# Optimization experiments

Hardware: AMD Instinct MI355X
Metric: run time of the kernel (lower is better)

## Reference

```python
import jax, jax.numpy as jnp
import numpy as np

NP_, NT_, NG_ = 110000, 20000, 10000  # node counts per relation graph
E = 500000                              # number of interaction records / edges
D = 64                                  # embedding_dim
F_USER, F_ITEM = 16, 16                 # engineered feature dims
NUM_LAYERS = (2, 2, 2)                  # CFG.feature_num_layers


def setup_inputs() -> dict:
    key = jax.random.key(0)
    ks = jax.random.split(key, 12)
    up_edge = jax.random.randint(ks[0], (2, E), 0, NP_, dtype=jnp.int32)
    ut_edge = jax.random.randint(ks[1], (2, E), 0, NT_, dtype=jnp.int32)
    utag_edge = jax.random.randint(ks[2], (2, E), 0, NG_, dtype=jnp.int32)
    src_feat = jax.random.normal(ks[3], (E, F_USER), dtype=jnp.float32)
    dst_feat = jax.random.normal(ks[4], (E, F_ITEM), dtype=jnp.float32)
    # xavier-uniform style embedding tables
    def xavier(k, shape):
        bound = np.sqrt(6.0 / (shape[0] + shape[1])).astype(np.float32)
        return jax.random.uniform(k, shape, jnp.float32, -bound, bound)
    up_emb = xavier(ks[5], (NP_, D))
    ut_emb = xavier(ks[6], (NT_, D))
    utag_emb = xavier(ks[7], (NG_, D))
    # feature-engineering linears (stored as [in, out]; torch does x @ W.T + b)
    W_src = jax.random.normal(ks[8], (F_USER, D), dtype=jnp.float32) / np.sqrt(F_USER)
    b_src = jnp.zeros((D,), jnp.float32)
    W_dst = jax.random.normal(ks[9], (F_ITEM, D), dtype=jnp.float32) / np.sqrt(F_ITEM)
    b_dst = jnp.zeros((D,), jnp.float32)
    return dict(up_edge=up_edge, ut_edge=ut_edge, utag_edge=utag_edge,
                src_feat=src_feat, dst_feat=dst_feat,
                up_emb=up_emb, ut_emb=ut_emb, utag_emb=utag_emb,
                W_src=W_src, b_src=b_src, W_dst=W_dst, b_dst=b_dst)


def lgconv(x, edge, n):
    # PyG LGConv: symmetric-normalized propagation, no self loops, no weights.
    src, dst = edge[0], edge[1]
    ones = jnp.ones(src.shape, x.dtype)
    deg = jax.ops.segment_sum(ones, dst, num_segments=n)
    dinv = jnp.where(deg > 0, jax.lax.rsqrt(jnp.maximum(deg, 1.0)), 0.0)
    norm = dinv[src] * dinv[dst]                      # [E]
    msg = x[src] * norm[:, None]                      # gather + scale  [E, D]
    return jax.ops.segment_sum(msg, dst, num_segments=n)  # scatter-add [N, D]


def propagate(emb, edge, n_layers):
    alpha = 1.0 / (n_layers + 1)
    x = emb
    out = emb * alpha
    for _ in range(n_layers):
        x = lgconv(x, edge, emb.shape[0])
        out = out + x * alpha
    return out


def reference(up_edge, ut_edge, utag_edge, src_feat, dst_feat,
              up_emb, ut_emb, utag_emb, W_src, b_src, W_dst, b_dst):
    fs = src_feat @ W_src + b_src                     # [E, D]
    fd = dst_feat @ W_dst + b_dst                     # [E, D]
    p = propagate(up_emb, up_edge, NUM_LAYERS[0])
    t = propagate(ut_emb, ut_edge, NUM_LAYERS[1])
    g = propagate(utag_emb, utag_edge, NUM_LAYERS[2])
    # feature_aggregation_method == 0 (sum method)
    out_src = (p[up_edge[0]] + t[ut_edge[0]] + g[utag_edge[0]]) * (1.0 / 3.0) + fs
    out_dst = (p[up_edge[1]] + t[ut_edge[1]] + g[utag_edge[1]]) * (1.0 / 3.0) + fd
    return (out_src * out_dst).sum(axis=-1)           # [E] link logits
```

## Files before the change

kernel.cpp:

```cpp
#include <hip/hip_runtime.h>

#define DIM 64
#define RNG 8
#define CHK 16
#define LDSH 14336

typedef __attribute__((ext_vector_type(4))) short s16x4;
typedef __attribute__((ext_vector_type(4))) float f32x4v;

__device__ __forceinline__ float bf2f(unsigned short u) {
    union { unsigned int i; float f; } v; v.i = ((unsigned int)u) << 16; return v.f;
}
__device__ __forceinline__ unsigned short f2bf(float f) {
    union { float f; unsigned int i; } v; v.f = f;
    unsigned int r = v.i + 0x7fff + ((v.i >> 16) & 1);
    return (unsigned short)(r >> 16);
}
__device__ __forceinline__ float4 u2f4(ushort4 u) {
    float4 f; f.x = bf2f(u.x); f.y = bf2f(u.y); f.z = bf2f(u.z); f.w = bf2f(u.w);
    return f;
}
__device__ __forceinline__ ushort4 f2u4(float4 f) {
    ushort4 u; u.x = f2bf(f.x); u.y = f2bf(f.y); u.z = f2bf(f.z); u.w = f2bf(f.w);
    return u;
}
__device__ __forceinline__ float4 fma4(float4 a, float s, float4 c) {
    c.x = fmaf(a.x, s, c.x); c.y = fmaf(a.y, s, c.y);
    c.z = fmaf(a.z, s, c.z); c.w = fmaf(a.w, s, c.w);
    return c;
}
__device__ __forceinline__ float4 add4(float4 a, float4 b) {
    float4 r; r.x = a.x + b.x; r.y = a.y + b.y; r.z = a.z + b.z; r.w = a.w + b.w;
    return r;
}

__global__ __launch_bounds__(1024) void deg_cvt_kernel(
        const int* __restrict__ up, const int* __restrict__ ut,
        const int* __restrict__ ug, int* __restrict__ hist,
        const float4* __restrict__ e0, const float4* __restrict__ e1,
        const float4* __restrict__ e2, ushort4* __restrict__ embh,
        const float* __restrict__ W_s, const float* __restrict__ W_d,
        s16x4* __restrict__ wfrag,
        int NP, int NT, int NG, int NTOT, int E) {
    __shared__ int lh[LDSH];
    int b = blockIdx.x;
    const int HB = 3 * RNG * CHK;
    if (b < HB) {
        int c  = b & (CHK - 1);
        int gr = b >> 4;
        int g  = gr >> 3;
        int r  = gr & (RNG - 1);
        const int* edge = (g == 0) ? up : (g == 1) ? ut : ug;
        int nb = (g == 0) ? 0 : (g == 1) ? NP : NP + NT;
        int Ng = (g == 0) ? NP : (g == 1) ? NT : NG;
        int Q  = (Ng + RNG - 1) / RNG;
        int lo = r * Q;
        int hi = lo + Q; if (hi > Ng) hi = Ng;
        int nloc = hi - lo;
        for (int t = threadIdx.x; t < nloc; t += 1024) lh[t] = 0;
        __syncthreads();
        int CE = (E + CHK - 1) / CHK;
        int jb = c * CE, je = jb + CE; if (je > E) je = E;
        for (int j = jb + threadIdx.x; j < je; j += 1024) {
            int t = edge[E + j];
            if (t >= lo && t < hi) atomicAdd(&lh[t - lo], 1);
        }
        __syncthreads();
        for (int t = threadIdx.x; t < nloc; t += 1024)
            hist[(size_t)c * NTOT + nb + lo + t] = lh[t];
        return;
    }
    int convBlocks = (NTOT * 16 + 1023) / 1024;
    if (b >= HB + convBlocks) {
        int i = threadIdx.x;
        if (i < 512) {
            int m = i >> 8;
            int t = (i >> 6) & 3;
            int l = i & 63;
            int q = l >> 4, cc = l & 15;
            const float* Wm = m ? W_d : W_s;
            s16x4 v;
#pragma unroll
            for (int j = 0; j < 4; ++j)
                v[j] = (short)f2bf(Wm[(4 * q + j) * 64 + 4 * cc + t]);
            wfrag[i] = v;
        }
        return;
    }
    int i2 = (b - HB) * 1024 + threadIdx.x;
    int np16 = NP * 16, nt16 = NT * 16, ng16 = NG * 16;
    if (i2 >= np16 + nt16 + ng16) return;
    const float4* s; int j;
    if (i2 < np16)              { s = e0; j = i2; }
    else if (i2 < np16 + nt16)  { s = e1; j = i2 - np16; }
    else                        { s = e2; j = i2 - np16 - nt16; }
    embh[i2] = f2u4(s[j]);
}

__global__ void sumdeg_kernel(const int* __restrict__ hist, int* __restrict__ csum,
                              int* __restrict__ deg, int n) {
    int i = blockIdx.x * 256 + threadIdx.x;
    if (i >= n) return;
    int run = 0;
#pragma unroll
    for (int c = 0; c < CHK; ++c) {
        csum[(size_t)c * n + i] = run;
        run += hist[(size_t)c * n + i];
    }
    deg[i] = run;
}

__global__ void block_sums(const int* __restrict__ deg, int* __restrict__ bsum,
                           int n) {
    int i = blockIdx.x * 256 + threadIdx.x;
    int v = (i < n) ? deg[i] : 0;
#pragma unroll
    for (int s = 1; s < 64; s <<= 1) v += __shfl_xor(v, s, 64);
    __shared__ int ws[4];
    if ((threadIdx.x & 63) == 0) ws[threadIdx.x >> 6] = v;
    __syncthreads();
    if (threadIdx.x == 0) bsum[blockIdx.x] = ws[0] + ws[1] + ws[2] + ws[3];
}

__global__ void scan_bsums(int* __restrict__ bsum, int nb) {
    int lane = threadIdx.x & 63, wid = threadIdx.x >> 6;
    int v = (threadIdx.x < nb) ? bsum[threadIdx.x] : 0;
    int x = v;
#pragma unroll
    for (int s = 1; s < 64; s <<= 1) {
        int y = __shfl_up(x, s, 64);
        if (lane >= s) x += y;
    }
    __shared__ int ws[16];
    if (lane == 63) ws[wid] = x;
    __syncthreads();
    int pre = 0;
    for (int w2 = 0; w2 < wid; ++w2) pre += ws[w2];
    if (threadIdx.x < nb) bsum[threadIdx.x] = pre + x - v;
}

__global__ void scatter_offs(const int* __restrict__ deg, const int* __restrict__ bpre,
                             int* __restrict__ offs, float* __restrict__ dinv,
                             int n, int total) {
    int i = blockIdx.x * 256 + threadIdx.x;
    int lane = threadIdx.x & 63, wid = threadIdx.x >> 6;
    int v = (i < n) ? deg[i] : 0;
    int x = v;
#pragma unroll
    for (int s = 1; s < 64; s <<= 1) {
        int y = __shfl_up(x, s, 64);
        if (lane >= s) x += y;
    }
    __shared__ int ws[4];
    if (lane == 63) ws[wid] = x;
    __syncthreads();
    int pre = bpre[blockIdx.x];
    for (int w2 = 0; w2 < wid; ++w2) pre += ws[w2];
    if (i < n) {
        int e = pre + x - v;
        offs[i] = e;
        dinv[i] = (v > 0) ? rsqrtf((float)v) : 0.0f;
    }
    if (i == 0) offs[n] = total;
}

__global__ __launch_bounds__(1024) void permute3_kernel(
        const int* __restrict__ up, const int* __restrict__ ut,
        const int* __restrict__ ug, const int* __restrict__ offs,
        const int* __restrict__ csum, int* __restrict__ ei,
        int NP, int NT, int NG, int NTOT, int E) {
    __shared__ int lcur[LDSH];
    int b = blockIdx.x;
    int c  = b / 24;
    int gr = b - c * 24;
    int g  = gr >> 3;
    int r  = gr & (RNG - 1);
    const int* edge = (g == 0) ? up : (g == 1) ? ut : ug;
    int nb = (g == 0) ? 0 : (g == 1) ? NP : NP + NT;
    int Ng = (g == 0) ? NP : (g == 1) ? NT : NG;
    int Q  = (Ng + RNG - 1) / RNG;
    int lo = r * Q;
    int hi = lo + Q; if (hi > Ng) hi = Ng;
    int nloc = hi - lo;
    for (int t = threadIdx.x; t < nloc; t += 1024)
        lcur[t] = offs[nb + lo + t] + csum[(size_t)c * NTOT + nb + lo + t];
    __syncthreads();
    int CE = (E + CHK - 1) / CHK;
    int jb = c * CE, je = jb + CE; if (je > E) je = E;
    for (int j = jb + threadIdx.x; j < je; j += 1024) {
        int t = edge[E + j];
        if (t >= lo && t < hi) {
            int p = atomicAdd(&lcur[t - lo], 1);
            ei[p] = edge[j] + nb;
        }
    }
}

__global__ void conv_csr1(const int* __restrict__ offs, const int* __restrict__ ei,
                          const float* __restrict__ dinv,
                          const ushort4* __restrict__ xin, ushort4* __restrict__ xout, int N) {
    int gid = blockIdx.x * blockDim.x + threadIdx.x;
    int n = gid >> 4, l = gid & 15;
    if (n >= N) return;
    int beg = offs[n], end = offs[n + 1];
    float4 a0 = {0.f, 0.f, 0.f, 0.f}, a1 = a0, a2 = a0, a3 = a0;
    int k = beg;
    for (; k + 3 < end; k += 4) {
        int s0 = ei[k], s1 = ei[k + 1], s2 = ei[k + 2], s3 = ei[k + 3];
        float w0 = dinv[s0], w1 = dinv[s1], w2 = dinv[s2], w3 = dinv[s3];
        ushort4 u0 = xin[(size_t)s0 * 16 + l];
        ushort4 u1 = xin[(size_t)s1 * 16 + l];
        ushort4 u2 = xin[(size_t)s2 * 16 + l];
        ushort4 u3 = xin[(size_t)s3 * 16 + l];
        a0 = fma4(u2f4(u0), w0, a0);
        a1 = fma4(u2f4(u1), w1, a1);
        a2 = fma4(u2f4(u2), w2, a2);
        a3 = fma4(u2f4(u3), w3, a3);
    }
    for (; k < end; ++k) {
        int s = ei[k];
        a0 = fma4(u2f4(xin[(size_t)s * 16 + l]), dinv[s], a0);
    }
    float4 acc = add4(add4(a0, a1), add4(a2, a3));
    float sc = dinv[n];
    float4 r; r.x = acc.x * sc; r.y = acc.y * sc; r.z = acc.z * sc; r.w = acc.w * sc;
    xout[(size_t)n * 16 + l] = f2u4(r);
}

__global__ void conv_csr2(const int* __restrict__ offs, const int* __restrict__ ei,
                          const float* __restrict__ dinv,
                          const ushort4* __restrict__ emb, const ushort4* __restrict__ x1,
                          ushort4* __restrict__ out, int N) {
    int gid = blockIdx.x * blockDim.x + threadIdx.x;
    int n = gid >> 4, l = gid & 15;
    if (n >= N) return;
    int beg = offs[n], end = offs[n + 1];
    float4 a0 = {0.f, 0.f, 0.f, 0.f}, a1 = a0, a2 = a0, a3 = a0;
    int k = beg;
    for (; k + 3 < end; k += 4) {
        int s0 = ei[k], s1 = ei[k + 1], s2 = ei[k + 2], s3 = ei[k + 3];
        float w0 = dinv[s0], w1 = dinv[s1], w2 = dinv[s2], w3 = dinv[s3];
        ushort4 u0 = x1[(size_t)s0 * 16 + l];
        ushort4 u1 = x1[(size_t)s1 * 16 + l];
        ushort4 u2 = x1[(size_t)s2 * 16 + l];
        ushort4 u3 = x1[(size_t)s3 * 16 + l];
        a0 = fma4(u2f4(u0), w0, a0);
        a1 = fma4(u2f4(u1), w1, a1);
        a2 = fma4(u2f4(u2), w2, a2);
        a3 = fma4(u2f4(u3), w3, a3);
    }
    for (; k < end; ++k) {
        int s = ei[k];
        a0 = fma4(u2f4(x1[(size_t)s * 16 + l]), dinv[s], a0);
    }
    float4 acc = add4(add4(a0, a1), add4(a2, a3));
    float sc = dinv[n];
    size_t idx = (size_t)n * 16 + l;
    float4 em = u2f4(emb[idx]), x = u2f4(x1[idx]);
    const float third = 1.0f / 3.0f;
    float4 o;
    o.x = (em.x + x.x + acc.x * sc) * third;
    o.y = (em.y + x.y + acc.y * sc) * third;
    o.z = (em.z + x.z + acc.z * sc) * third;
    o.w = (em.w + x.w + acc.w * sc) * third;
    out[idx] = f2u4(o);
}

__global__ __launch_bounds__(256) void final_kernel(
        const int* __restrict__ up_e, const int* __restrict__ ut_e,
        const int* __restrict__ utag_e,
        const float* __restrict__ src_feat, const float* __restrict__ dst_feat,
        const ushort4* __restrict__ O, const s16x4* __restrict__ wfrag,
        const float4* __restrict__ b_s4, const float4* __restrict__ b_d4,
        float* __restrict__ out, int E, int NP, int NT) {
    int tid = threadIdx.x;
    int wv = tid >> 6;
    int l  = tid & 63;
    int c  = l & 15;
    int q  = l >> 4;
    int e0w = (blockIdx.x * 4 + wv) * 16;
    if (e0w >= E) return;

    int ea = e0w + c; if (ea > E - 1) ea = E - 1;
    float4 fa = *(const float4*)(src_feat + (size_t)ea * 16 + q * 4);
    float4 ga = *(const float4*)(dst_feat + (size_t)ea * 16 + q * 4);

    s16x4 Bs[4], Bd[4];
#pragma unroll
    for (int t = 0; t < 4; ++t) {
        Bs[t] = wfrag[t * 64 + l];
        Bd[t] = wfrag[256 + t * 64 + l];
    }
    float4 bsv = b_s4[c], bdv = b_d4[c];

    s16x4 As, Ad;
    As[0] = (short)f2bf(fa.x); As[1] = (short)f2bf(fa.y);
    As[2] = (short)f2bf(fa.z); As[3] = (short)f2bf(fa.w);
    Ad[0] = (short)f2bf(ga.x); Ad[1] = (short)f2bf(ga.y);
    Ad[2] = (short)f2bf(ga.z); Ad[3] = (short)f2bf(ga.w);

    ushort4 as[4][3], bs[4][3];
#pragma unroll
    for (int r = 0; r < 4; ++r) {
        int e = e0w + q * 4 + r; if (e > E - 1) e = E - 1;
        int sp = up_e[e],             dp = up_e[E + e];
        int st = ut_e[e] + NP,        dt = ut_e[E + e] + NP;
        int sg = utag_e[e] + NP + NT, dg = utag_e[E + e] + NP + NT;
        as[r][0] = O[(size_t)sp * 16 + c];
        as[r][1] = O[(size_t)st * 16 + c];
        as[r][2] = O[(size_t)sg * 16 + c];
        bs[r][0] = O[(size_t)dp * 16 + c];
        bs[r][1] = O[(size_t)dt * 16 + c];
        bs[r][2] = O[(size_t)dg * 16 + c];
    }
    __builtin_amdgcn_sched_barrier(0);

    f32x4v Cs[4], Cd[4];
    f32x4v zz = {0.f, 0.f, 0.f, 0.f};
#pragma unroll
    for (int t = 0; t < 4; ++t) {
        Cs[t] = __builtin_amdgcn_mfma_f32_16x16x16bf16_1k(As, Bs[t], zz, 0, 0, 0);
        Cd[t] = __builtin_amdgcn_mfma_f32_16x16x16bf16_1k(Ad, Bd[t], zz, 0, 0, 0);
    }

    const float third = 1.0f / 3.0f;
#pragma unroll
    for (int r = 0; r < 4; ++r) {
        int er = e0w + q * 4 + r;
        float4 fsv, fdv;
        fsv.x = Cs[0][r] + bsv.x; fsv.y = Cs[1][r] + bsv.y;
        fsv.z = Cs[2][r] + bsv.z; fsv.w = Cs[3][r] + bsv.w;
        fdv.x = Cd[0][r] + bdv.x; fdv.y = Cd[1][r] + bdv.y;
        fdv.z = Cd[2][r] + bdv.z; fdv.w = Cd[3][r] + bdv.w;
        float4 vp = u2f4(as[r][0]), vt = u2f4(as[r][1]), vg = u2f4(as[r][2]);
        float4 P, Q;
        P.x = (vp.x + vt.x + vg.x) * third + fsv.x;
        P.y = (vp.y + vt.y + vg.y) * third + fsv.y;
        P.z = (vp.z + vt.z + vg.z) * third + fsv.z;
        P.w = (vp.w + vt.w + vg.w) * third + fsv.w;
        vp = u2f4(bs[r][0]); vt = u2f4(bs[r][1]); vg = u2f4(bs[r][2]);
        Q.x = (vp.x + vt.x + vg.x) * third + fdv.x;
        Q.y = (vp.y + vt.y + vg.y) * third + fdv.y;
        Q.z = (vp.z + vt.z + vg.z) * third + fdv.z;
        Q.w = (vp.w + vt.w + vg.w) * third + fdv.w;
        float p = P.x * Q.x + P.y * Q.y + P.z * Q.z + P.w * Q.w;
        p += __shfl_xor(p, 8, 64);
        p += __shfl_xor(p, 4, 64);
        p += __shfl_xor(p, 2, 64);
        p += __shfl_xor(p, 1, 64);
        if (c == 0 && er < E) out[er] = p;
    }
}

extern "C" void kernel_launch(void* const* d_in, const int* in_sizes, int n_in,
                              void* d_out, int out_size, void* d_ws, size_t ws_size,
                              hipStream_t stream) {
    const int*   up_e     = (const int*)d_in[0];
    const int*   ut_e     = (const int*)d_in[1];
    const int*   utag_e   = (const int*)d_in[2];
    const float* src_feat = (const float*)d_in[3];
    const float* dst_feat = (const float*)d_in[4];
    const float* up_emb   = (const float*)d_in[5];
    const float* ut_emb   = (const float*)d_in[6];
    const float* utag_emb = (const float*)d_in[7];
    const float* W_src    = (const float*)d_in[8];
    const float* b_src    = (const float*)d_in[9];
    const float* W_dst    = (const float*)d_in[10];
    const float* b_dst    = (const float*)d_in[11];
    float* out = (float*)d_out;

    const int E  = in_sizes[0] / 2;
    const int NP = in_sizes[5] / DIM;
    const int NT = in_sizes[6] / DIM;
    const int NG = in_sizes[7] / DIM;
    const int NTOT = NP + NT + NG;
    const int NB = (NTOT + 255) / 256;

    char* w = (char*)d_ws;
    int*  hist = (int*)w;                       w += (size_t)CHK * NTOT * 4;
    int*  csum = (int*)w;                       w += (size_t)CHK * NTOT * 4;
    int*  deg  = (int*)w;                       w += (size_t)NTOT * 4;
    int*  offs = (int*)w;                       w += (size_t)(NTOT + 1) * 4;
    int*  bsum = (int*)w;                       w += (size_t)1024 * 4;
    float* dinv = (float*)w;                    w += (size_t)NTOT * 4;
    w = (char*)(((uintptr_t)w + 127) & ~(uintptr_t)127);
    s16x4* wfrag = (s16x4*)w;                   w += (size_t)512 * 8;
    w = (char*)(((uintptr_t)w + 127) & ~(uintptr_t)127);
    int*  ei   = (int*)w;                       w += (size_t)3 * E * 4;
    w = (char*)(((uintptr_t)w + 127) & ~(uintptr_t)127);
    ushort4* embh = (ushort4*)w;                w += (size_t)NTOT * 16 * 8;
    ushort4* x1h  = (ushort4*)w;                w += (size_t)NTOT * 16 * 8;
    ushort4* outh = (ushort4*)w;

    const int BT = 256;
    const int HB = 3 * RNG * CHK;

    {
        int convBlocks = (NTOT * 16 + 1023) / 1024;
        deg_cvt_kernel<<<dim3(HB + convBlocks + 1), dim3(1024), 0, stream>>>(
            up_e, ut_e, utag_e, hist,
            (const float4*)up_emb, (const float4*)ut_emb, (const float4*)utag_emb,
            embh, W_src, W_dst, wfrag, NP, NT, NG, NTOT, E);
    }

    sumdeg_kernel<<<dim3(NB), dim3(BT), 0, stream>>>(hist, csum, deg, NTOT);

    block_sums<<<dim3(NB), dim3(BT), 0, stream>>>(deg, bsum, NTOT);
    scan_bsums<<<dim3(1), dim3(1024), 0, stream>>>(bsum, NB);
    scatter_offs<<<dim3(NB), dim3(BT), 0, stream>>>(deg, bsum, offs, dinv, NTOT, 3 * E);

    permute3_kernel<<<dim3(CHK * 24), dim3(1024), 0, stream>>>(
        up_e, ut_e, utag_e, offs, csum, ei, NP, NT, NG, NTOT, E);

    int nb = ((size_t)NTOT * 16 + BT - 1) / BT;
    conv_csr1<<<dim3(nb), dim3(BT), 0, stream>>>(offs, ei, dinv, embh, x1h, NTOT);
    conv_csr2<<<dim3(nb), dim3(BT), 0, stream>>>(offs, ei, dinv, embh, x1h, outh, NTOT);

    {
        int blocks = (E + 63) / 64;
        final_kernel<<<dim3(blocks), dim3(BT), 0, stream>>>(
            up_e, ut_e, utag_e, src_feat, dst_feat, outh, wfrag,
            (const float4*)b_src, (const float4*)b_dst, out, E, NP, NT);
    }
}
```

Measured before the change: 329.1 us.

## Software-pipeline final kernel over four edge tiles and unroll CSR gather loops by eight

The final kernel now has each wave handle 64 edges as four 16-edge tiles. While the current tile's embedding gathers and MFMA run, it prefetches the edge indices and features for the next tile, and it loads the weight fragments once per wave instead of once per 16 edges. Separately, both CSR convolution kernels get an 8-way unrolled gather loop so more loads are in flight per thread. The cost is fewer blocks in the final kernel, which lowers parallelism, plus higher register pressure in all three kernels.

```diff
diff --git a/kernel.cpp b/kernel.cpp
--- a/kernel.cpp
+++ b/kernel.cpp
@@ -4,6 +4,7 @@
 #define RNG 8
 #define CHK 16
 #define LDSH 14336
+#define EPT 64
 
 typedef __attribute__((ext_vector_type(4))) short s16x4;
 typedef __attribute__((ext_vector_type(4))) float f32x4v;
@@ -205,6 +206,28 @@
     int beg = offs[n], end = offs[n + 1];
     float4 a0 = {0.f, 0.f, 0.f, 0.f}, a1 = a0, a2 = a0, a3 = a0;
     int k = beg;
+    for (; k + 7 < end; k += 8) {
+        int s0 = ei[k], s1 = ei[k + 1], s2 = ei[k + 2], s3 = ei[k + 3];
+        int s4 = ei[k + 4], s5 = ei[k + 5], s6 = ei[k + 6], s7 = ei[k + 7];
+        float w0 = dinv[s0], w1 = dinv[s1], w2 = dinv[s2], w3 = dinv[s3];
+        float w4 = dinv[s4], w5 = dinv[s5], w6 = dinv[s6], w7 = dinv[s7];
+        ushort4 u0 = xin[(size_t)s0 * 16 + l];
+        ushort4 u1 = xin[(size_t)s1 * 16 + l];
+        ushort4 u2 = xin[(size_t)s2 * 16 + l];
+        ushort4 u3 = xin[(size_t)s3 * 16 + l];
+        ushort4 u4 = xin[(size_t)s4 * 16 + l];
+        ushort4 u5 = xin[(size_t)s5 * 16 + l];
+        ushort4 u6 = xin[(size_t)s6 * 16 + l];
+        ushort4 u7 = xin[(size_t)s7 * 16 + l];
+        a0 = fma4(u2f4(u0), w0, a0);
+        a1 = fma4(u2f4(u1), w1, a1);
+        a2 = fma4(u2f4(u2), w2, a2);
+        a3 = fma4(u2f4(u3), w3, a3);
+        a0 = fma4(u2f4(u4), w4, a0);
+        a1 = fma4(u2f4(u5), w5, a1);
+        a2 = fma4(u2f4(u6), w6, a2);
+        a3 = fma4(u2f4(u7), w7, a3);
+    }
     for (; k + 3 < end; k += 4) {
         int s0 = ei[k], s1 = ei[k + 1], s2 = ei[k + 2], s3 = ei[k + 3];
         float w0 = dinv[s0], w1 = dinv[s1], w2 = dinv[s2], w3 = dinv[s3];
@@ -237,6 +260,28 @@
     int beg = offs[n], end = offs[n + 1];
     float4 a0 = {0.f, 0.f, 0.f, 0.f}, a1 = a0, a2 = a0, a3 = a0;
     int k = beg;
+    for (; k + 7 < end; k += 8) {
+        int s0 = ei[k], s1 = ei[k + 1], s2 = ei[k + 2], s3 = ei[k + 3];
+        int s4 = ei[k + 4], s5 = ei[k + 5], s6 = ei[k + 6], s7 = ei[k + 7];
+        float w0 = dinv[s0], w1 = dinv[s1], w2 = dinv[s2], w3 = dinv[s3];
+        float w4 = dinv[s4], w5 = dinv[s5], w6 = dinv[s6], w7 = dinv[s7];
+        ushort4 u0 = x1[(size_t)s0 * 16 + l];
+        ushort4 u1 = x1[(size_t)s1 * 16 + l];
+        ushort4 u2 = x1[(size_t)s2 * 16 + l];
+        ushort4 u3 = x1[(size_t)s3 * 16 + l];
+        ushort4 u4 = x1[(size_t)s4 * 16 + l];
+        ushort4 u5 = x1[(size_t)s5 * 16 + l];
+        ushort4 u6 = x1[(size_t)s6 * 16 + l];
+        ushort4 u7 = x1[(size_t)s7 * 16 + l];
+        a0 = fma4(u2f4(u0), w0, a0);
+        a1 = fma4(u2f4(u1), w1, a1);
+        a2 = fma4(u2f4(u2), w2, a2);
+        a3 = fma4(u2f4(u3), w3, a3);
+        a0 = fma4(u2f4(u4), w4, a0);
+        a1 = fma4(u2f4(u5), w5, a1);
+        a2 = fma4(u2f4(u6), w6, a2);
+        a3 = fma4(u2f4(u7), w7, a3);
+    }
     for (; k + 3 < end; k += 4) {
         int s0 = ei[k], s1 = ei[k + 1], s2 = ei[k + 2], s3 = ei[k + 3];
         float w0 = dinv[s0], w1 = dinv[s1], w2 = dinv[s2], w3 = dinv[s3];
@@ -278,12 +323,8 @@
     int l  = tid & 63;
     int c  = l & 15;
     int q  = l >> 4;
-    int e0w = (blockIdx.x * 4 + wv) * 16;
-    if (e0w >= E) return;
-
-    int ea = e0w + c; if (ea > E - 1) ea = E - 1;
-    float4 fa = *(const float4*)(src_feat + (size_t)ea * 16 + q * 4);
-    float4 ga = *(const float4*)(dst_feat + (size_t)ea * 16 + q * 4);
+    int wbase = (blockIdx.x * 4 + wv) * EPT;
+    if (wbase >= E) return;
 
     s16x4 Bs[4], Bd[4];
 #pragma unroll
@@ -292,63 +333,90 @@
         Bd[t] = wfrag[256 + t * 64 + l];
     }
     float4 bsv = b_s4[c], bdv = b_d4[c];
-
-    s16x4 As, Ad;
-    As[0] = (short)f2bf(fa.x); As[1] = (short)f2bf(fa.y);
-    As[2] = (short)f2bf(fa.z); As[3] = (short)f2bf(fa.w);
-    Ad[0] = (short)f2bf(ga.x); Ad[1] = (short)f2bf(ga.y);
-    Ad[2] = (short)f2bf(ga.z); Ad[3] = (short)f2bf(ga.w);
-
-    ushort4 as[4][3], bs[4][3];
+    const float third = 1.0f / 3.0f;
+
+    int ea = wbase + c; if (ea > E - 1) ea = E - 1;
+    float4 fa = *(const float4*)(src_feat + (size_t)ea * 16 + q * 4);
+    float4 ga = *(const float4*)(dst_feat + (size_t)ea * 16 + q * 4);
+    int isp[4], idp[4], ist[4], idt[4], isg[4], idg[4];
 #pragma unroll
     for (int r = 0; r < 4; ++r) {
-        int e = e0w + q * 4 + r; if (e > E - 1) e = E - 1;
-        int sp = up_e[e],             dp = up_e[E + e];
-        int st = ut_e[e] + NP,        dt = ut_e[E + e] + NP;
-        int sg = utag_e[e] + NP + NT, dg = utag_e[E + e] + NP + NT;
-        as[r][0] = O[(size_t)sp * 16 + c];
-        as[r][1] = O[(size_t)st * 16 + c];
-        as[r][2] = O[(size_t)sg * 16 + c];
-        bs[r][0] = O[(size_t)dp * 16 + c];
-        bs[r][1] = O[(size_t)dt * 16 + c];
-        bs[r][2] = O[(size_t)dg * 16 + c];
-    }
-    __builtin_amdgcn_sched_barrier(0);
-
-    f32x4v Cs[4], Cd[4];
-    f32x4v zz = {0.f, 0.f, 0.f, 0.f};
-#pragma unroll
+        int e = wbase + q * 4 + r; if (e > E - 1) e = E - 1;
+        isp[r] = up_e[e];             idp[r] = up_e[E + e];
+        ist[r] = ut_e[e] + NP;        idt[r] = ut_e[E + e] + NP;
+        isg[r] = utag_e[e] + NP + NT; idg[r] = utag_e[E + e] + NP + NT;
+    }
+
     for (int t = 0; t < 4; ++t) {
-        Cs[t] = __builtin_amdgcn_mfma_f32_16x16x16bf16_1k(As, Bs[t], zz, 0, 0, 0);
-        Cd[t] = __builtin_amdgcn_mfma_f32_16x16x16bf16_1k(Ad, Bd[t], zz, 0, 0, 0);
-    }
-
-    const float third = 1.0f / 3.0f;
-#pragma unroll
-    for (int r = 0; r < 4; ++r) {
-        int er = e0w + q * 4 + r;
-        float4 fsv, fdv;
-        fsv.x = Cs[0][r] + bsv.x; fsv.y = Cs[1][r] + bsv.y;
-        fsv.z = Cs[2][r] + bsv.z; fsv.w = Cs[3][r] + bsv.w;
-        fdv.x = Cd[0][r] + bdv.x; fdv.y = Cd[1][r] + bdv.y;
-        fdv.z = Cd[2][r] + bdv.z; fdv.w = Cd[3][r] + bdv.w;
-        float4 vp = u2f4(as[r][0]), vt = u2f4(as[r][1]), vg = u2f4(as[r][2]);
-        float4 P, Q;
-        P.x = (vp.x + vt.x + vg.x) * third + fsv.x;
-        P.y = (vp.y + vt.y + vg.y) * third + fsv.y;
-        P.z = (vp.z + vt.z + vg.z) * third + fsv.z;
-        P.w = (vp.w + vt.w + vg.w) * third + fsv.w;
-        vp = u2f4(bs[r][0]); vt = u2f4(bs[r][1]); vg = u2f4(bs[r][2]);
-        Q.x = (vp.x + vt.x + vg.x) * third + fdv.x;
-        Q.y = (vp.y + vt.y + vg.y) * third + fdv.y;
-        Q.z = (vp.z + vt.z + vg.z) * third + fdv.z;
-        Q.w = (vp.w + vt.w + vg.w) * third + fdv.w;
-        float p = P.x * Q.x + P.y * Q.y + P.z * Q.z + P.w * Q.w;
-        p += __shfl_xor(p, 8, 64);
-        p += __shfl_xor(p, 4, 64);
-        p += __shfl_xor(p, 2, 64);
-        p += __shfl_xor(p, 1, 64);
-        if (c == 0 && er < E) out[er] = p;
+        int tb = wbase + t * 16;
+        if (tb >= E) break;
+
+        ushort4 as[4][3], bs[4][3];
+#pragma unroll
+        for (int r = 0; r < 4; ++r) {
+            as[r][0] = O[(size_t)isp[r] * 16 + c];
+            as[r][1] = O[(size_t)ist[r] * 16 + c];
+            as[r][2] = O[(size_t)isg[r] * 16 + c];
+            bs[r][0] = O[(size_t)idp[r] * 16 + c];
+            bs[r][1] = O[(size_t)idt[r] * 16 + c];
+            bs[r][2] = O[(size_t)idg[r] * 16 + c];
+        }
+
+        s16x4 As, Ad;
+        As[0] = (short)f2bf(fa.x); As[1] = (short)f2bf(fa.y);
+        As[2] = (short)f2bf(fa.z); As[3] = (short)f2bf(fa.w);
+        Ad[0] = (short)f2bf(ga.x); Ad[1] = (short)f2bf(ga.y);
+        Ad[2] = (short)f2bf(ga.z); Ad[3] = (short)f2bf(ga.w);
+
+        int nb2 = tb + 16;
+        if (t < 3 && nb2 < E) {
+            int ea2 = nb2 + c; if (ea2 > E - 1) ea2 = E - 1;
+            fa = *(const float4*)(src_feat + (size_t)ea2 * 16 + q * 4);
+            ga = *(const float4*)(dst_feat + (size_t)ea2 * 16 + q * 4);
+#pragma unroll
+            for (int r = 0; r < 4; ++r) {
+                int e = nb2 + q * 4 + r; if (e > E - 1) e = E - 1;
+                isp[r] = up_e[e];             idp[r] = up_e[E + e];
+                ist[r] = ut_e[e] + NP;        idt[r] = ut_e[E + e] + NP;
+                isg[r] = utag_e[e] + NP + NT; idg[r] = utag_e[E + e] + NP + NT;
+            }
+        }
+        __builtin_amdgcn_sched_barrier(0);
+
+        f32x4v Cs[4], Cd[4];
+        f32x4v zz = {0.f, 0.f, 0.f, 0.f};
+#pragma unroll
+        for (int tt = 0; tt < 4; ++tt) {
+            Cs[tt] = __builtin_amdgcn_mfma_f32_16x16x16bf16_1k(As, Bs[tt], zz, 0, 0, 0);
+            Cd[tt] = __builtin_amdgcn_mfma_f32_16x16x16bf16_1k(Ad, Bd[tt], zz, 0, 0, 0);
+        }
+
+#pragma unroll
+        for (int r = 0; r < 4; ++r) {
+            int er = tb + q * 4 + r;
+            float4 fsv, fdv;
+            fsv.x = Cs[0][r] + bsv.x; fsv.y = Cs[1][r] + bsv.y;
+            fsv.z = Cs[2][r] + bsv.z; fsv.w = Cs[3][r] + bsv.w;
+            fdv.x = Cd[0][r] + bdv.x; fdv.y = Cd[1][r] + bdv.y;
+            fdv.z = Cd[2][r] + bdv.z; fdv.w = Cd[3][r] + bdv.w;
+            float4 vp = u2f4(as[r][0]), vt = u2f4(as[r][1]), vg = u2f4(as[r][2]);
+            float4 P, Q;
+            P.x = (vp.x + vt.x + vg.x) * third + fsv.x;
+            P.y = (vp.y + vt.y + vg.y) * third + fsv.y;
+            P.z = (vp.z + vt.z + vg.z) * third + fsv.z;
+            P.w = (vp.w + vt.w + vg.w) * third + fsv.w;
+            vp = u2f4(bs[r][0]); vt = u2f4(bs[r][1]); vg = u2f4(bs[r][2]);
+            Q.x = (vp.x + vt.x + vg.x) * third + fdv.x;
+            Q.y = (vp.y + vt.y + vg.y) * third + fdv.y;
+            Q.z = (vp.z + vt.z + vg.z) * third + fdv.z;
+            Q.w = (vp.w + vt.w + vg.w) * third + fdv.w;
+            float p = P.x * Q.x + P.y * Q.y + P.z * Q.z + P.w * Q.w;
+            p += __shfl_xor(p, 8, 64);
+            p += __shfl_xor(p, 4, 64);
+            p += __shfl_xor(p, 2, 64);
+            p += __shfl_xor(p, 1, 64);
+            if (c == 0 && er < E) out[er] = p;
+        }
     }
 }
 
@@ -417,7 +485,7 @@
     conv_csr2<<<dim3(nb), dim3(BT), 0, stream>>>(offs, ei, dinv, embh, x1h, outh, NTOT);
 
     {
-        int blocks = (E + 63) / 64;
+        int blocks = (E + 4 * EPT - 1) / (4 * EPT);
         final_kernel<<<dim3(blocks), dim3(BT), 0, stream>>>(
             up_e, ut_e, utag_e, src_feat, dst_feat, outh, wfrag,
             (const float4*)b_src, (const float4*)b_dst, out, E, NP, NT);
```

Measured after the change: 350.0 us. +6.4%, slower.
